# Performance work log

Measured on AMD Instinct MI355X. Metric: run time of the kernel, lower is better.

Reference implementation:

```python
import jax, jax.numpy as jnp
import numpy as np
from math import sqrt

B = 32          # batch
C = 81          # label_num (class 0 = background, skipped)
N = 15130       # number of default boxes
K = 200         # max_num candidates per class
MAX_OUT = 200   # max_output boxes per image
SCORE_THR = 0.05
CRITERIA = 0.45
SCALE_XY = 0.1
SCALE_WH = 0.2
NEG_INF = -1e30


def make_dboxes_xywh():
    """Replicates DefaultBoxes for figsize (1200,1200), SSD-R34 COCO config."""
    fig = 1200
    feat = [50, 25, 13, 7, 3, 3]
    scales = [int(s * fig / 300) for s in [21, 45, 99, 153, 207, 261, 315]]
    aspect_ratios = [[2], [2, 3], [2, 3], [2, 3], [2], [2]]
    boxes = []
    for idx, f in enumerate(feat):
        step = int(fig / f)
        fk = fig // step  # == f for this config
        sk1 = scales[idx] / fig
        sk2 = scales[idx + 1] / fig
        sk3 = sqrt(sk1 * sk2)
        sizes = [(sk1, sk1), (sk3, sk3)]
        for a in aspect_ratios[idx]:
            w, h = sk1 * sqrt(a), sk1 / sqrt(a)
            sizes.append((w, h))
            sizes.append((h, w))
        for (w, h) in sizes:
            for i in range(f):
                for j in range(f):
                    cx, cy = (j + 0.5) / fk, (i + 0.5) / fk
                    boxes.append((cx, cy, w, h))
    d = np.clip(np.array(boxes, dtype=np.float32), 0.0, 1.0)
    assert d.shape[0] == N
    return d[None, :, :]  # [1, N, 4]


def setup_inputs() -> dict:
    key = jax.random.key(0)
    k1, k2 = jax.random.split(key)
    bboxes_in = jax.random.normal(k1, (B, 4, N), dtype=jnp.float32)
    scores_in = jax.random.normal(k2, (B, C, N), dtype=jnp.float32)
    dboxes_xywh = jnp.asarray(make_dboxes_xywh())
    return {"bboxes_in": bboxes_in, "scores_in": scores_in, "dboxes_xywh": dboxes_xywh}


def scale_back_batch(bboxes_in, scores_in, dboxes_xywh):
    b = jnp.transpose(bboxes_in, (0, 2, 1))            # [B, N, 4]
    xy = SCALE_XY * b[..., :2] * dboxes_xywh[..., 2:] + dboxes_xywh[..., :2]
    wh = jnp.exp(SCALE_WH * b[..., 2:]) * dboxes_xywh[..., 2:]
    ltrb = jnp.concatenate([xy - 0.5 * wh, xy + 0.5 * wh], axis=-1)  # [B, N, 4]
    probs = jax.nn.softmax(jnp.transpose(scores_in, (0, 2, 1)), axis=-1)  # [B, N, C]
    return ltrb, probs


def pairwise_iou(b):
    """Faithful to calc_iou_tensor: the masked_fill_ on delta.clone() is a no-op
    in the original, so negative deltas are NOT clamped."""
    lt = jnp.maximum(b[:, None, :2], b[None, :, :2])
    rb = jnp.minimum(b[:, None, 2:], b[None, :, 2:])
    d = rb - lt
    inter = d[..., 0] * d[..., 1]
    area = (b[:, 2] - b[:, 0]) * (b[:, 3] - b[:, 1])
    return inter / (area[:, None] + area[None, :] - inter)  # [K, K]


def nms_one_class(boxes, score):
    """boxes [N,4], score [N] -> kept boxes [K,4], kept scores [K] (NEG_INF = dropped).
    Greedy NMS over the top-K scores in descending order, matching the original
    while-loop (ascending sort + pop-from-end)."""
    s = jnp.where(score > SCORE_THR, score, NEG_INF)
    top_s, top_i = jax.lax.top_k(s, K)         # descending
    bk = boxes[top_i]                          # [K, 4]
    iou = pairwise_iou(bk)                     # [K, K]
    rng = jnp.arange(K)
    keep0 = top_s > NEG_INF

    def body(i, keep):
        suppress = keep[i] & (iou[i] >= CRITERIA) & (rng > i)
        return keep & ~suppress

    keep = jax.lax.fori_loop(0, K, body, keep0)
    return bk, jnp.where(keep, top_s, NEG_INF)


def decode_image(boxes, probs):
    """boxes [N,4], probs [N,C] -> (boxes [MAX_OUT,4], labels [MAX_OUT], scores [MAX_OUT])."""
    cls_scores = jnp.transpose(probs[:, 1:])                    # [C-1, N] (skip background)
    bks, ss = jax.vmap(nms_one_class, in_axes=(None, 0))(boxes, cls_scores)  # [C-1,K,4],[C-1,K]
    labels = jnp.repeat(jnp.arange(1, C, dtype=jnp.int32), K)   # [(C-1)*K]
    flat_s = ss.reshape(-1)
    top_s, top_i = jax.lax.top_k(flat_s, MAX_OUT)               # global top max_output
    out_boxes = bks.reshape(-1, 4)[top_i]
    out_labels = labels[top_i]
    valid = top_s > NEG_INF
    return (jnp.where(valid[:, None], out_boxes, 0.0),
            jnp.where(valid, out_labels, 0),
            jnp.where(valid, top_s, 0.0))


def reference(bboxes_in, scores_in, dboxes_xywh):
    ltrb, probs = scale_back_batch(bboxes_in, scores_in, dboxes_xywh)
    boxes, labels, scores = jax.vmap(decode_image)(ltrb, probs)
    return boxes, labels, scores  # [B,MAX_OUT,4], [B,MAX_OUT] int32, [B,MAX_OUT]
```

## Files before the change

### kernel.cpp

```cpp
#include <hip/hip_runtime.h>
#include <cstdint>
#include <cstddef>

#define BATCH 32
#define NCLS 81
#define NFG 80
#define NBOX 15130
#define NCHUNK 60
#define TOPK 200
#define NTASK (BATCH * NFG)
#define NEG_INF -1e30f
#define GCAP 1024
#define SORTCAP 1024
#define LCAP 4864
#define SCORE_THR 0.05f
#define CRITERIA 0.45f

__global__ __launch_bounds__(256) void k1_fused(
    const float* __restrict__ bboxes,
    const float* __restrict__ scores,
    const float* __restrict__ dboxes,
    float4* __restrict__ ltrb,
    unsigned long long* __restrict__ gcand,
    int* __restrict__ gcnt)
{
    const int blk = blockIdx.x;
    const int b = blk / NCHUNK;
    const int chunk = blk - b * NCHUNK;
    const int tid = threadIdx.x;
    const int n = chunk * 256 + tid;

    __shared__ unsigned long long list[LCAP];
    __shared__ int lcnt;
    __shared__ int ccnt[NFG];
    __shared__ int cbase[NFG];

    if (tid == 0) lcnt = 0;
    if (tid < NFG) ccnt[tid] = 0;
    __syncthreads();

    float m = 0.f, s = 1.f, thrv = 1e30f;
    const float* sc = scores;

    if (n < NBOX) {
        const float* bb = bboxes + (size_t)b * 4 * NBOX + n;
        float bx = bb[0];
        float by = bb[NBOX];
        float bw = bb[2 * (size_t)NBOX];
        float bh = bb[3 * (size_t)NBOX];
        float4 d = reinterpret_cast<const float4*>(dboxes)[n];
        float xx = __fadd_rn(__fmul_rn(__fmul_rn(0.1f, bx), d.z), d.x);
        float yy = __fadd_rn(__fmul_rn(__fmul_rn(0.1f, by), d.w), d.y);
        float wx = __fmul_rn(expf(__fmul_rn(0.2f, bw)), d.z);
        float wy = __fmul_rn(expf(__fmul_rn(0.2f, bh)), d.w);
        float4 o;
        o.x = __fsub_rn(xx, __fmul_rn(0.5f, wx));
        o.y = __fsub_rn(yy, __fmul_rn(0.5f, wy));
        o.z = __fadd_rn(xx, __fmul_rn(0.5f, wx));
        o.w = __fadd_rn(yy, __fmul_rn(0.5f, wy));
        ltrb[(size_t)b * NBOX + n] = o;

        sc = scores + (size_t)b * NCLS * NBOX + n;
        {
            float vals[NCLS];
#pragma unroll
            for (int c = 0; c < NCLS; ++c) vals[c] = sc[(size_t)c * NBOX];
            m = vals[0];
#pragma unroll
            for (int c = 1; c < NCLS; ++c) m = fmaxf(m, vals[c]);
            float ss = 0.0f;
#pragma unroll
            for (int c = 0; c < NCLS; ++c) ss = __fadd_rn(ss, expf(__fsub_rn(vals[c], m)));
            s = ss;
        }
        thrv = __fsub_rn(__fadd_rn(m, logf(__fmul_rn(0.05f, s))), 1e-3f);
    }

    if (n < NBOX) {
        uintptr_t scu = (uintptr_t)sc;
        asm volatile("" : "+v"(scu));
        const float* scv = (const float*)scu;
        for (int c0 = 1; c0 < NCLS; c0 += 16) {
            float vt[16];
#pragma unroll
            for (int u = 0; u < 16; ++u) {
                int c = c0 + u;
                vt[u] = (c < NCLS) ? scv[(size_t)c * NBOX] : -1e30f;
            }
#pragma unroll
            for (int u = 0; u < 16; ++u) {
                int c = c0 + u;
                if (vt[u] > thrv) {
                    float p = __fdiv_rn(expf(__fsub_rn(vt[u], m)), s);
                    if (p > SCORE_THR) {
                        int e = atomicAdd(&lcnt, 1);
                        if (e < LCAP)
                            list[e] = ((unsigned long long)__float_as_uint(p) << 32) |
                                      ((unsigned long long)(unsigned)(c - 1) << 24) |
                                      (unsigned long long)(unsigned)n;
                    }
                }
            }
        }
    }
    __syncthreads();

    const int E = min(lcnt, LCAP);

    for (int i = tid; i < E; i += 256) {
        int c = (int)((list[i] >> 24) & 0xFF);
        atomicAdd(&ccnt[c], 1);
    }
    __syncthreads();

    if (tid < NFG && ccnt[tid] > 0)
        cbase[tid] = atomicAdd(&gcnt[b * NFG + tid], ccnt[tid]);
    __syncthreads();
    if (tid < NFG) ccnt[tid] = 0;
    __syncthreads();

    for (int i = tid; i < E; i += 256) {
        unsigned long long e = list[i];
        int c = (int)((e >> 24) & 0xFF);
        unsigned nn = (unsigned)(e & 0xFFFFFF);
        int pos = cbase[c] + atomicAdd(&ccnt[c], 1);
        if (pos < GCAP) {
            unsigned pb = (unsigned)(e >> 32);
            gcand[(size_t)(b * NFG + c) * GCAP + pos] =
                ((unsigned long long)pb << 32) |
                (unsigned long long)(0xFFFFFFFFu - nn);
        }
    }
}

template<int J, int K>
__device__ __forceinline__ void bstep(unsigned long long (&it)[16], const int lane) {
    if constexpr (J >= 64) {
        constexpr int M = J >> 6;
#pragma unroll
        for (int r = 0; r < 16; ++r) {
            const int rp = r ^ M;
            if (rp > r) {
                const bool desc = (((unsigned)(r << 6) & (unsigned)K) == 0u);
                unsigned long long a = it[r], bb = it[rp];
                if (desc ? (a < bb) : (a > bb)) { it[r] = bb; it[rp] = a; }
            }
        }
    } else {
#pragma unroll
        for (int r = 0; r < 16; ++r) {
            unsigned long long a = it[r];
            unsigned long long bb = __shfl_xor(a, J, 64);
            const unsigned i = ((unsigned)(r << 6)) | (unsigned)lane;
            const bool desc = ((i & (unsigned)K) == 0u);
            const bool lower = ((lane & J) == 0);
            it[r] = ((desc == lower) ? (a >= bb) : (a <= bb)) ? a : bb;
        }
    }
}

template<int K, int J>
__device__ __forceinline__ void bstage(unsigned long long (&it)[16], const int lane) {
    bstep<J, K>(it, lane);
    if constexpr (J > 1) bstage<K, (J >> 1)>(it, lane);
}

__global__ __launch_bounds__(64) void k2_nms(
    const unsigned long long* __restrict__ gcand,
    const int* __restrict__ gcnt,
    const float4* __restrict__ ltrb,
    float* __restrict__ cls_scores,
    int* __restrict__ cls_idx)
{
    const int t = blockIdx.x;
    const int b = t / NFG;
    const int lane = threadIdx.x;

    __shared__ float4 sbox[TOPK];
    __shared__ float sarea[TOPK];

    const int cl = min(gcnt[t], SORTCAP);
    const unsigned long long* gc = gcand + (size_t)t * GCAP;

    unsigned long long it[16];
#pragma unroll
    for (int r = 0; r < 16; ++r) {
        const int i = (r << 6) + lane;
        it[r] = (i < cl) ? gc[i] : 0ULL;
    }

    unsigned kmax = 2;
    while (kmax < (unsigned)cl) kmax <<= 1;

    bstage<2, 1>(it, lane);
    if (kmax >= 4)    bstage<4, 2>(it, lane);
    if (kmax >= 8)    bstage<8, 4>(it, lane);
    if (kmax >= 16)   bstage<16, 8>(it, lane);
    if (kmax >= 32)   bstage<32, 16>(it, lane);
    if (kmax >= 64)   bstage<64, 32>(it, lane);
    if (kmax >= 128)  bstage<128, 64>(it, lane);
    if (kmax >= 256)  bstage<256, 128>(it, lane);
    if (kmax >= 512)  bstage<512, 256>(it, lane);
    if (kmax >= 1024) bstage<1024, 512>(it, lane);

    const int mk = min(cl, TOPK);

    float4 myb[4];
    float mya[4], myp[4];
    int myn[4];
#pragma unroll
    for (int r = 0; r < 4; ++r) {
        const int i = (r << 6) + lane;
        myb[r] = make_float4(0.f, 0.f, 0.f, 0.f);
        mya[r] = 0.f; myp[r] = 0.f; myn[r] = 0;
        if (i < mk) {
            const unsigned long long key = it[r];
            const unsigned n = 0xFFFFFFFFu - (unsigned)(key & 0xFFFFFFFFull);
            const float4 bx = ltrb[(size_t)b * NBOX + n];
            myb[r] = bx;
            mya[r] = __fmul_rn(__fsub_rn(bx.z, bx.x), __fsub_rn(bx.w, bx.y));
            myp[r] = __uint_as_float((unsigned)(key >> 32));
            myn[r] = b * NBOX + (int)n;
            sbox[i] = bx;
            sarea[i] = mya[r];
        }
    }
    __syncthreads();

    auto maskBits = [](int r) -> unsigned long long {
        if (r <= 0) return 0ULL;
        if (r >= 64) return ~0ULL;
        return (1ULL << r) - 1ULL;
    };
    unsigned long long kw0 = maskBits(mk);
    unsigned long long kw1 = maskBits(mk - 64);
    unsigned long long kw2 = maskBits(mk - 128);
    unsigned long long kw3 = maskBits(mk - 192);

#define NMS_QUAD(KWQ, Q)                                                           \
    {                                                                              \
        const int i0 = (Q) << 6;                                                   \
        const int i1 = min(mk, i0 + 64);                                           \
        for (int i = i0; i < i1; ++i) {                                            \
            if ((KWQ >> (i - i0)) & 1ULL) {                                        \
                const float4 bi = sbox[i];                                         \
                const float ai = sarea[i];                                         \
                _Pragma("unroll")                                                  \
                for (int q2 = 0; q2 < 4; ++q2) {                                   \
                    const int j = (q2 << 6) + lane;                                \
                    const float4 bj = myb[q2];                                     \
                    const float ltx = fmaxf(bi.x, bj.x), lty = fmaxf(bi.y, bj.y);  \
                    const float rbx = fminf(bi.z, bj.z), rby = fminf(bi.w, bj.w);  \
                    const float dx = __fsub_rn(rbx, ltx), dy = __fsub_rn(rby, lty);\
                    const float inter = __fmul_rn(dx, dy);                         \
                    const float uni = __fsub_rn(__fadd_rn(ai, mya[q2]), inter);    \
                    const float iou = __fdiv_rn(inter, uni);                       \
                    const unsigned long long sup =                                 \
                        __ballot((iou >= CRITERIA) && (j > i));                    \
                    if (q2 == 0) kw0 &= ~sup;                                      \
                    else if (q2 == 1) kw1 &= ~sup;                                 \
                    else if (q2 == 2) kw2 &= ~sup;                                 \
                    else kw3 &= ~sup;                                              \
                }                                                                  \
            }                                                                      \
        }                                                                          \
    }
    NMS_QUAD(kw0, 0)
    NMS_QUAD(kw1, 1)
    NMS_QUAD(kw2, 2)
    NMS_QUAD(kw3, 3)
#undef NMS_QUAD

#pragma unroll
    for (int r = 0; r < 4; ++r) {
        const int i = (r << 6) + lane;
        if (i < TOPK) {
            const unsigned long long kq = (r == 0) ? kw0 : (r == 1) ? kw1
                                         : (r == 2) ? kw2 : kw3;
            const bool keep = (i < mk) && ((kq >> lane) & 1ULL);
            cls_scores[(size_t)t * TOPK + i] = keep ? myp[r] : NEG_INF;
            if (i < mk) cls_idx[(size_t)t * TOPK + i] = myn[r];
        }
    }
}

__device__ __forceinline__ int blockReduceSum(int x, int* red, int tid) {
    __syncthreads();
    red[tid] = x;
    __syncthreads();
    for (int off = 128; off > 0; off >>= 1) {
        if (tid < off) red[tid] += red[tid + off];
        __syncthreads();
    }
    return red[0];
}

__global__ __launch_bounds__(256) void k3_topk(
    const float* __restrict__ cls_scores,
    const int* __restrict__ cls_idx,
    const float4* __restrict__ ltrb,
    float* __restrict__ out)
{
    const int b = blockIdx.x;
    const int tid = threadIdx.x;
    const int NFLAT = NFG * TOPK;
    const int PER = 63;

    __shared__ unsigned long long sel[512];
    __shared__ int scnt;
    __shared__ int red[256];

    const float* S = cls_scores + (size_t)b * NFLAT;
    float v[PER];
#pragma unroll
    for (int i = 0; i < PER; ++i) {
        int j = i * 256 + tid;
        v[i] = (j < NFLAT) ? S[j] : NEG_INF;
    }

    int lc = 0;
#pragma unroll
    for (int i = 0; i < PER; ++i) lc += (v[i] > -1e29f) ? 1 : 0;
    int validCount = blockReduceSum(lc, red, tid);

    unsigned thrBits = 0;
    if (validCount > TOPK) {
        unsigned lo = 0, hi = 0x7F800000u;
        while (lo < hi) {
            unsigned mid = (lo + hi) >> 1;
            float mf = __uint_as_float(mid);
            int c2 = 0;
#pragma unroll
            for (int i = 0; i < PER; ++i) c2 += (v[i] > mf) ? 1 : 0;
            int tot = blockReduceSum(c2, red, tid);
            if (tot < TOPK) hi = mid; else lo = mid + 1;
        }
        thrBits = lo;
    }

    __syncthreads();
    if (tid == 0) scnt = 0;
    for (int i = tid; i < 512; i += 256) sel[i] = 0ULL;
    __syncthreads();

    const bool useGE = (validCount > TOPK);
    const float thrF = __uint_as_float(thrBits);
#pragma unroll
    for (int i = 0; i < PER; ++i) {
        int j = i * 256 + tid;
        bool take = useGE ? (v[i] >= thrF) : (v[i] > -1e29f);
        if (j < NFLAT && take) {
            int pos = atomicAdd(&scnt, 1);
            if (pos < 512) {
                sel[pos] = ((unsigned long long)__float_as_uint(v[i]) << 32) |
                           (unsigned long long)(0xFFFFFFFFu - (unsigned)j);
            }
        }
    }
    __syncthreads();
    int total = min(min(scnt, 512), TOPK);

    for (unsigned k = 2; k <= 512; k <<= 1) {
        for (unsigned j = k >> 1; j > 0; j >>= 1) {
            for (unsigned i = tid; i < 512; i += 256) {
                unsigned ixj = i ^ j;
                if (ixj > i) {
                    unsigned long long a = sel[i], bb2 = sel[ixj];
                    bool desc = ((i & k) == 0);
                    if (desc ? (a < bb2) : (a > bb2)) { sel[i] = bb2; sel[ixj] = a; }
                }
            }
            __syncthreads();
        }
    }

    if (tid < TOPK) {
        size_t ob = (size_t)b * TOPK + tid;
        float4 bx = make_float4(0.f, 0.f, 0.f, 0.f);
        float lab = 0.f, sc2 = 0.f;
        if (tid < total) {
            unsigned long long key = sel[tid];
            unsigned j = 0xFFFFFFFFu - (unsigned)(key & 0xFFFFFFFFull);
            sc2 = __uint_as_float((unsigned)(key >> 32));
            unsigned cls = j / TOPK;
            int gi = cls_idx[(size_t)b * NFLAT + j];
            bx = ltrb[gi];
            lab = (float)(cls + 1);
        }
        reinterpret_cast<float4*>(out)[ob] = bx;
        out[(size_t)BATCH * TOPK * 4 + ob] = lab;
        out[(size_t)BATCH * TOPK * 4 + (size_t)BATCH * TOPK + ob] = sc2;
    }
}

extern "C" void kernel_launch(void* const* d_in, const int* in_sizes, int n_in,
                              void* d_out, int out_size, void* d_ws, size_t ws_size,
                              hipStream_t stream) {
    (void)in_sizes; (void)n_in; (void)out_size; (void)ws_size;
    const float* bboxes = (const float*)d_in[0];
    const float* scores = (const float*)d_in[1];
    const float* dboxes = (const float*)d_in[2];
    float* out = (float*)d_out;

    char* ws = (char*)d_ws;
    size_t off = 0;
    float4* ltrb = (float4*)(ws + off);      off += (size_t)BATCH * NBOX * 16;
    unsigned long long* gcand = (unsigned long long*)(ws + off);
                                             off += (size_t)NTASK * GCAP * 8;
    float* cls_scores = (float*)(ws + off);  off += (size_t)NTASK * TOPK * 4;
    int*   cls_idx    = (int*)(ws + off);    off += (size_t)NTASK * TOPK * 4;
    int*   gcnt       = (int*)(ws + off);    off += (size_t)NTASK * 4;

    hipMemsetAsync(gcnt, 0, NTASK * sizeof(int), stream);

    k1_fused<<<BATCH * NCHUNK, 256, 0, stream>>>(bboxes, scores, dboxes, ltrb, gcand, gcnt);
    k2_nms<<<NTASK, 64, 0, stream>>>(gcand, gcnt, ltrb, cls_scores, cls_idx);
    k3_topk<<<BATCH, 256, 0, stream>>>(cls_scores, cls_idx, ltrb, out);
}
```

Before: 231.7 us.

## Shrink k1 shared list with global overflow, size-specialize k2 sort, prefetch NMS boxes

In k1, the shared candidate list shrinks from 4864 to 1920 entries, and any overflow is written straight to the global per-class candidate buffers through global atomics. This cuts shared memory per block so more blocks can be resident. In k2, the bitonic sort is templated on register count, so small candidate counts (up to 256 or 512) sort with 4 or 8 registers instead of 16, which lowers register pressure and skips stages. The NMS loop also software-prefetches the next box and area from LDS. The risk is divergent code paths and more global atomic traffic whenever a chunk overflows.

```diff
diff --git a/kernel.cpp b/kernel.cpp
--- a/kernel.cpp
+++ b/kernel.cpp
@@ -12,7 +12,7 @@
 #define NEG_INF -1e30f
 #define GCAP 1024
 #define SORTCAP 1024
-#define LCAP 4864
+#define LCAP 1920
 #define SCORE_THR 0.05f
 #define CRITERIA 0.45f
 
@@ -94,10 +94,17 @@
                     float p = __fdiv_rn(expf(__fsub_rn(vt[u], m)), s);
                     if (p > SCORE_THR) {
                         int e = atomicAdd(&lcnt, 1);
-                        if (e < LCAP)
+                        if (e < LCAP) {
                             list[e] = ((unsigned long long)__float_as_uint(p) << 32) |
                                       ((unsigned long long)(unsigned)(c - 1) << 24) |
                                       (unsigned long long)(unsigned)n;
+                        } else {
+                            int pos = atomicAdd(&gcnt[b * NFG + (c - 1)], 1);
+                            if (pos < GCAP)
+                                gcand[(size_t)(b * NFG + (c - 1)) * GCAP + pos] =
+                                    ((unsigned long long)__float_as_uint(p) << 32) |
+                                    (unsigned long long)(0xFFFFFFFFu - (unsigned)n);
+                        }
                     }
                 }
             }
@@ -133,12 +140,12 @@
     }
 }
 
-template<int J, int K>
-__device__ __forceinline__ void bstep(unsigned long long (&it)[16], const int lane) {
+template<int NR, int J, int K>
+__device__ __forceinline__ void bstep(unsigned long long (&it)[NR], const int lane) {
     if constexpr (J >= 64) {
         constexpr int M = J >> 6;
 #pragma unroll
-        for (int r = 0; r < 16; ++r) {
+        for (int r = 0; r < NR; ++r) {
             const int rp = r ^ M;
             if (rp > r) {
                 const bool desc = (((unsigned)(r << 6) & (unsigned)K) == 0u);
@@ -148,7 +155,7 @@
         }
     } else {
 #pragma unroll
-        for (int r = 0; r < 16; ++r) {
+        for (int r = 0; r < NR; ++r) {
             unsigned long long a = it[r];
             unsigned long long bb = __shfl_xor(a, J, 64);
             const unsigned i = ((unsigned)(r << 6)) | (unsigned)lane;
@@ -159,10 +166,27 @@
     }
 }
 
-template<int K, int J>
-__device__ __forceinline__ void bstage(unsigned long long (&it)[16], const int lane) {
-    bstep<J, K>(it, lane);
-    if constexpr (J > 1) bstage<K, (J >> 1)>(it, lane);
+template<int NR, int K, int J>
+__device__ __forceinline__ void bstage(unsigned long long (&it)[NR], const int lane) {
+    bstep<NR, J, K>(it, lane);
+    if constexpr (J > 1) bstage<NR, K, (J >> 1)>(it, lane);
+}
+
+template<int NR>
+__device__ __forceinline__ void bsort(unsigned long long (&it)[NR], const int lane,
+                                      const unsigned kmax) {
+    bstage<NR, 2, 1>(it, lane);
+    if (kmax >= 4)   bstage<NR, 4, 2>(it, lane);
+    if (kmax >= 8)   bstage<NR, 8, 4>(it, lane);
+    if (kmax >= 16)  bstage<NR, 16, 8>(it, lane);
+    if (kmax >= 32)  bstage<NR, 32, 16>(it, lane);
+    if (kmax >= 64)  bstage<NR, 64, 32>(it, lane);
+    if constexpr (NR >= 4) {
+        if (kmax >= 128) bstage<NR, 128, 64>(it, lane);
+        if (kmax >= 256) bstage<NR, 256, 128>(it, lane);
+    }
+    if constexpr (NR >= 8)  { if (kmax >= 512)  bstage<NR, 512, 256>(it, lane); }
+    if constexpr (NR >= 16) { if (kmax >= 1024) bstage<NR, 1024, 512>(it, lane); }
 }
 
 __global__ __launch_bounds__(64) void k2_nms(
@@ -182,26 +206,41 @@
     const int cl = min(gcnt[t], SORTCAP);
     const unsigned long long* gc = gcand + (size_t)t * GCAP;
 
-    unsigned long long it[16];
-#pragma unroll
-    for (int r = 0; r < 16; ++r) {
-        const int i = (r << 6) + lane;
-        it[r] = (i < cl) ? gc[i] : 0ULL;
-    }
-
     unsigned kmax = 2;
     while (kmax < (unsigned)cl) kmax <<= 1;
 
-    bstage<2, 1>(it, lane);
-    if (kmax >= 4)    bstage<4, 2>(it, lane);
-    if (kmax >= 8)    bstage<8, 4>(it, lane);
-    if (kmax >= 16)   bstage<16, 8>(it, lane);
-    if (kmax >= 32)   bstage<32, 16>(it, lane);
-    if (kmax >= 64)   bstage<64, 32>(it, lane);
-    if (kmax >= 128)  bstage<128, 64>(it, lane);
-    if (kmax >= 256)  bstage<256, 128>(it, lane);
-    if (kmax >= 512)  bstage<512, 256>(it, lane);
-    if (kmax >= 1024) bstage<1024, 512>(it, lane);
+    unsigned long long top4[4];
+    if (cl <= 256) {
+        unsigned long long it[4];
+#pragma unroll
+        for (int r = 0; r < 4; ++r) {
+            const int i = (r << 6) + lane;
+            it[r] = (i < cl) ? gc[i] : 0ULL;
+        }
+        bsort<4>(it, lane, kmax);
+#pragma unroll
+        for (int r = 0; r < 4; ++r) top4[r] = it[r];
+    } else if (cl <= 512) {
+        unsigned long long it[8];
+#pragma unroll
+        for (int r = 0; r < 8; ++r) {
+            const int i = (r << 6) + lane;
+            it[r] = (i < cl) ? gc[i] : 0ULL;
+        }
+        bsort<8>(it, lane, kmax);
+#pragma unroll
+        for (int r = 0; r < 4; ++r) top4[r] = it[r];
+    } else {
+        unsigned long long it[16];
+#pragma unroll
+        for (int r = 0; r < 16; ++r) {
+            const int i = (r << 6) + lane;
+            it[r] = (i < cl) ? gc[i] : 0ULL;
+        }
+        bsort<16>(it, lane, kmax);
+#pragma unroll
+        for (int r = 0; r < 4; ++r) top4[r] = it[r];
+    }
 
     const int mk = min(cl, TOPK);
 
@@ -214,7 +253,7 @@
         myb[r] = make_float4(0.f, 0.f, 0.f, 0.f);
         mya[r] = 0.f; myp[r] = 0.f; myn[r] = 0;
         if (i < mk) {
-            const unsigned long long key = it[r];
+            const unsigned long long key = top4[r];
             const unsigned n = 0xFFFFFFFFu - (unsigned)(key & 0xFFFFFFFFull);
             const float4 bx = ltrb[(size_t)b * NBOX + n];
             myb[r] = bx;
@@ -237,14 +276,20 @@
     unsigned long long kw2 = maskBits(mk - 128);
     unsigned long long kw3 = maskBits(mk - 192);
 
+    float4 nb = sbox[0];
+    float na = sarea[0];
+
 #define NMS_QUAD(KWQ, Q)                                                           \
     {                                                                              \
         const int i0 = (Q) << 6;                                                   \
         const int i1 = min(mk, i0 + 64);                                           \
         for (int i = i0; i < i1; ++i) {                                            \
+            const float4 bi = nb;                                                  \
+            const float ai = na;                                                   \
+            const int ip = min(i + 1, TOPK - 1);                                   \
+            nb = sbox[ip];                                                         \
+            na = sarea[ip];                                                        \
             if ((KWQ >> (i - i0)) & 1ULL) {                                        \
-                const float4 bi = sbox[i];                                         \
-                const float ai = sarea[i];                                         \
                 _Pragma("unroll")                                                  \
                 for (int q2 = 0; q2 < 4; ++q2) {                                   \
                     const int j = (q2 << 6) + lane;                                \
```

Result: faster. 209.1 us (-9.7%).
